# Kernel tuning notes

Hardware: AMD Instinct MI355X
Metric: run time of the kernel (lower is better)

The kernel has to match this reference:

```python
import jax, jax.numpy as jnp
import numpy as np

EPS = 1e-5


def setup_inputs() -> dict:
    key = jax.random.key(0)
    k1, k2 = jax.random.split(key)
    B, N = 8, 1024  # batch, max_num_atoms
    coords = jax.random.normal(k1, (B, 3 * N), dtype=jnp.float32) * 10.0
    num_atoms = jax.random.randint(k2, (B,), 512, N + 1, dtype=jnp.int64)
    return {"coords": coords, "num_atoms": num_atoms}


def reference(coords, num_atoms):
    # coords: [B, 3*N] flat, num_atoms: [B]
    B = coords.shape[0]
    N = coords.shape[1] // 3
    c = coords.reshape(B, N, 3)
    # validity mask replicating the zero-padding of sep_mat in the torch code
    valid = jnp.arange(N)[None, :] < num_atoms[:, None]            # [B, N]
    pair_mask = (valid[:, :, None] & valid[:, None, :]).astype(coords.dtype)  # [B, N, N]
    # pairwise separation vectors, zeroed outside the valid block
    sep = (c[:, :, None, :] - c[:, None, :, :]) * pair_mask[..., None]  # [B, N, N, 3]
    dist2 = jnp.sum(sep * sep, axis=-1) + EPS                        # [B, N, N]
    # off-diagonal 3x3 Hessian blocks: -sep \otimes sep / d^2
    hess = -(sep[..., :, None] * sep[..., None, :]) / dist2[..., None, None]  # [B, N, N, 3, 3]
    # diagonal blocks: negative row-sum over partner atoms
    # (for padded rows and the pre-overwrite diagonal, blocks are exactly 0,
    #  so setting the diagonal unconditionally matches the torch per-row loop)
    diag = -hess.sum(axis=2)                                         # [B, N, 3, 3]
    idx = jnp.arange(N)
    hess = hess.at[:, idx, idx].set(diag)
    # [B, N, N, 3, 3] -> [B, N, 3, N, 3] -> [B, 3N, 3N]
    hess = jnp.swapaxes(hess, 2, 3)
    return hess.reshape(B, 3 * N, 3 * N)
```

## Files before the change

### kernel.cpp

```cpp
#include <hip/hip_runtime.h>

#define EPS 1e-5f

__global__ __launch_bounds__(256) void c2s_kernel(
    const float* __restrict__ coords,
    const int*   __restrict__ num_atoms,
    float*       __restrict__ out,
    int N)
{
    const int i   = blockIdx.x;
    const int b   = blockIdx.y;
    const int tid = threadIdx.x;
    const int n3  = 3 * N;

    const float* cb = coords + (size_t)b * n3;
    const int na   = num_atoms[b];
    const bool vi  = (i < na);

    const float cix = cb[3 * i + 0];
    const float ciy = cb[3 * i + 1];
    const float ciz = cb[3 * i + 2];

    float sxx = 0.f, sxy = 0.f, sxz = 0.f, syy = 0.f, syz = 0.f, szz = 0.f;

    float* r0 = out + ((size_t)b * n3 + (size_t)(3 * i)) * n3;
    float* r1 = r0 + n3;
    float* r2 = r1 + n3;

    for (int j0 = 0; j0 < N; j0 += 256) {
        const int j = j0 + tid;
        const float m = (vi && (j < na)) ? 1.0f : 0.0f;
        const float dx = (cix - cb[3 * j + 0]) * m;
        const float dy = (ciy - cb[3 * j + 1]) * m;
        const float dz = (ciz - cb[3 * j + 2]) * m;
        const float inv = 1.0f / (dx * dx + dy * dy + dz * dz + EPS);
        const float hxx = dx * dx * inv, hxy = dx * dy * inv, hxz = dx * dz * inv;
        const float hyy = dy * dy * inv, hyz = dy * dz * inv, hzz = dz * dz * inv;
        sxx += hxx; sxy += hxy; sxz += hxz;
        syy += hyy; syz += hyz; szz += hzz;
        if (j != i) {
            r0[3 * j + 0] = -hxx; r0[3 * j + 1] = -hxy; r0[3 * j + 2] = -hxz;
            r1[3 * j + 0] = -hxy; r1[3 * j + 1] = -hyy; r1[3 * j + 2] = -hyz;
            r2[3 * j + 0] = -hxz; r2[3 * j + 1] = -hyz; r2[3 * j + 2] = -hzz;
        }
    }

    #pragma unroll
    for (int off = 32; off > 0; off >>= 1) {
        sxx += __shfl_down(sxx, off);
        sxy += __shfl_down(sxy, off);
        sxz += __shfl_down(sxz, off);
        syy += __shfl_down(syy, off);
        syz += __shfl_down(syz, off);
        szz += __shfl_down(szz, off);
    }
    __shared__ float red[4][6];
    const int wave = tid >> 6;
    const int lane = tid & 63;
    if (lane == 0) {
        red[wave][0] = sxx; red[wave][1] = sxy; red[wave][2] = sxz;
        red[wave][3] = syy; red[wave][4] = syz; red[wave][5] = szz;
    }
    __syncthreads();
    if (tid == 0) {
        const float dxx = red[0][0] + red[1][0] + red[2][0] + red[3][0];
        const float dxy = red[0][1] + red[1][1] + red[2][1] + red[3][1];
        const float dxz = red[0][2] + red[1][2] + red[2][2] + red[3][2];
        const float dyy = red[0][3] + red[1][3] + red[2][3] + red[3][3];
        const float dyz = red[0][4] + red[1][4] + red[2][4] + red[3][4];
        const float dzz = red[0][5] + red[1][5] + red[2][5] + red[3][5];
        r0[3 * i + 0] = dxx; r0[3 * i + 1] = dxy; r0[3 * i + 2] = dxz;
        r1[3 * i + 0] = dxy; r1[3 * i + 1] = dyy; r1[3 * i + 2] = dyz;
        r2[3 * i + 0] = dxz; r2[3 * i + 1] = dyz; r2[3 * i + 2] = dzz;
    }
}

extern "C" void kernel_launch(void* const* d_in, const int* in_sizes, int n_in,
                              void* d_out, int out_size, void* d_ws, size_t ws_size,
                              hipStream_t stream) {
    const float* coords    = (const float*)d_in[0];
    const int*   num_atoms = (const int*)d_in[1];
    float*       out       = (float*)d_out;

    const int B = in_sizes[1];
    const int N = in_sizes[0] / (3 * B);

    dim3 grid(N, B);
    c2s_kernel<<<grid, 256, 0, stream>>>(coords, num_atoms, out, N);
}
```

Before: 49.90 us.

## Stage Hessian rows in LDS and write out with 128-bit coalesced stores

Each block now writes its three output rows into shared memory (36 KB for N=1024), then copies them to global memory with 16-byte vector stores. This replaces the stride-3 scalar global stores, which coalesce poorly, with contiguous wide writes. It also swaps the exact division for the hardware reciprocal instruction. The cost is heavier LDS use, which lowers occupancy to a few blocks per CU, plus an extra barrier and an LDS round trip, and the approximate reciprocal changes rounding slightly.

```diff
diff --git a/kernel.cpp b/kernel.cpp
--- a/kernel.cpp
+++ b/kernel.cpp
@@ -1,6 +1,8 @@
 #include <hip/hip_runtime.h>
 
 #define EPS 1e-5f
+
+typedef float f32x4 __attribute__((ext_vector_type(4)));
 
 __global__ __launch_bounds__(256) void c2s_kernel(
     const float* __restrict__ coords,
@@ -8,6 +10,8 @@
     float*       __restrict__ out,
     int N)
 {
+    extern __shared__ float lds[];
+
     const int i   = blockIdx.x;
     const int b   = blockIdx.y;
     const int tid = threadIdx.x;
@@ -21,28 +25,24 @@
     const float ciy = cb[3 * i + 1];
     const float ciz = cb[3 * i + 2];
 
+    float* l0 = lds;
+    float* l1 = lds + n3;
+    float* l2 = lds + 2 * n3;
+
     float sxx = 0.f, sxy = 0.f, sxz = 0.f, syy = 0.f, syz = 0.f, szz = 0.f;
-
-    float* r0 = out + ((size_t)b * n3 + (size_t)(3 * i)) * n3;
-    float* r1 = r0 + n3;
-    float* r2 = r1 + n3;
-
-    for (int j0 = 0; j0 < N; j0 += 256) {
-        const int j = j0 + tid;
+    for (int j = tid; j < N; j += 256) {
         const float m = (vi && (j < na)) ? 1.0f : 0.0f;
         const float dx = (cix - cb[3 * j + 0]) * m;
         const float dy = (ciy - cb[3 * j + 1]) * m;
         const float dz = (ciz - cb[3 * j + 2]) * m;
-        const float inv = 1.0f / (dx * dx + dy * dy + dz * dz + EPS);
+        const float inv = __builtin_amdgcn_rcpf(dx * dx + dy * dy + dz * dz + EPS);
         const float hxx = dx * dx * inv, hxy = dx * dy * inv, hxz = dx * dz * inv;
         const float hyy = dy * dy * inv, hyz = dy * dz * inv, hzz = dz * dz * inv;
         sxx += hxx; sxy += hxy; sxz += hxz;
         syy += hyy; syz += hyz; szz += hzz;
-        if (j != i) {
-            r0[3 * j + 0] = -hxx; r0[3 * j + 1] = -hxy; r0[3 * j + 2] = -hxz;
-            r1[3 * j + 0] = -hxy; r1[3 * j + 1] = -hyy; r1[3 * j + 2] = -hyz;
-            r2[3 * j + 0] = -hxz; r2[3 * j + 1] = -hyz; r2[3 * j + 2] = -hzz;
-        }
+        l0[3 * j + 0] = -hxx; l0[3 * j + 1] = -hxy; l0[3 * j + 2] = -hxz;
+        l1[3 * j + 0] = -hxy; l1[3 * j + 1] = -hyy; l1[3 * j + 2] = -hyz;
+        l2[3 * j + 0] = -hxz; l2[3 * j + 1] = -hyz; l2[3 * j + 2] = -hzz;
     }
 
     #pragma unroll
@@ -69,10 +69,17 @@
         const float dyy = red[0][3] + red[1][3] + red[2][3] + red[3][3];
         const float dyz = red[0][4] + red[1][4] + red[2][4] + red[3][4];
         const float dzz = red[0][5] + red[1][5] + red[2][5] + red[3][5];
-        r0[3 * i + 0] = dxx; r0[3 * i + 1] = dxy; r0[3 * i + 2] = dxz;
-        r1[3 * i + 0] = dxy; r1[3 * i + 1] = dyy; r1[3 * i + 2] = dyz;
-        r2[3 * i + 0] = dxz; r2[3 * i + 1] = dyz; r2[3 * i + 2] = dzz;
+        l0[3 * i + 0] = dxx; l0[3 * i + 1] = dxy; l0[3 * i + 2] = dxz;
+        l1[3 * i + 0] = dxy; l1[3 * i + 1] = dyy; l1[3 * i + 2] = dyz;
+        l2[3 * i + 0] = dxz; l2[3 * i + 1] = dyz; l2[3 * i + 2] = dzz;
     }
+    __syncthreads();
+
+    f32x4*       dst = reinterpret_cast<f32x4*>(out + ((size_t)b * n3 + (size_t)(3 * i)) * n3);
+    const f32x4* src = reinterpret_cast<const f32x4*>(lds);
+    const int nf4 = (3 * n3) >> 2;
+    for (int f = tid; f < nf4; f += 256)
+        dst[f] = src[f];
 }
 
 extern "C" void kernel_launch(void* const* d_in, const int* in_sizes, int n_in,
@@ -86,5 +93,6 @@
     const int N = in_sizes[0] / (3 * B);
 
     dim3 grid(N, B);
-    c2s_kernel<<<grid, 256, 0, stream>>>(coords, num_atoms, out, N);
+    size_t shmem = (size_t)(3 * 3 * N) * sizeof(float);
+    c2s_kernel<<<grid, 256, shmem, stream>>>(coords, num_atoms, out, N);
 }
```

Result: slower. 55.78 us (+11.8%).
